# Performance work log

Hardware: AMD Instinct MI355X
Metric: run time of the kernel (lower is better)

The kernel has to match this reference:

```python
import jax, jax.numpy as jnp
import numpy as np

N_NODES = 100000

def gcn_conv(x, edge_index, W, b):
    # GCNConv with normalize=True and self-loops:
    # out = D^{-1/2} (A + I) D^{-1/2} (x W) + b
    h = x @ W                                   # [N, out]
    src, dst = edge_index[0], edge_index[1]
    deg = jax.ops.segment_sum(jnp.ones(src.shape[0], h.dtype), dst,
                              num_segments=N_NODES) + 1.0  # +1 for self loop
    dinv = jax.lax.rsqrt(deg)
    norm = dinv[src] * dinv[dst]                # [E]
    agg = jax.ops.segment_sum(h[src] * norm[:, None], dst,
                              num_segments=N_NODES)        # [N, out]
    agg = agg + h * (1.0 / deg)[:, None]        # self-loop term: norm_ii = 1/deg_i
    return agg + b


def setup_inputs() -> dict:
    key = jax.random.key(0)
    k0, k1, k2, k3 = jax.random.split(key, 4)
    N, E, F_IN, H, C = N_NODES, 1600000, 256, 128, 40
    x = jax.random.normal(k0, (N, F_IN), dtype=jnp.float32)
    edge_index = jax.random.randint(k1, (2, E), 0, N, dtype=jnp.int64)
    W1 = jax.random.normal(k2, (F_IN, H), dtype=jnp.float32) * (1.0 / np.sqrt(F_IN))
    b1 = jnp.zeros((H,), jnp.float32)
    W2 = jax.random.normal(k3, (H, C), dtype=jnp.float32) * (1.0 / np.sqrt(H))
    b2 = jnp.zeros((C,), jnp.float32)
    return {"x": x, "edge_index": edge_index, "W1": W1, "b1": b1, "W2": W2, "b2": b2}


def reference(x, edge_index, W1, b1, W2, b2):
    # layer 1 + ReLU (dropout = identity in eval mode)
    h = jax.nn.relu(gcn_conv(x, edge_index, W1, b1))
    # final layer (no activation)
    return gcn_conv(h, edge_index, W2, b2)
```

## Files before the change

kernel.cpp:

```cpp
#include <hip/hip_runtime.h>
#include <hip/hip_bf16.h>


#define FIN 256
#define HDIM 128
#define CDIM 40
#define CAP 8192
#define EC 8192

typedef __attribute__((ext_vector_type(8))) short bf16x8;
typedef __attribute__((ext_vector_type(4))) float f32x4;

__device__ inline short f2bf(float f) {
    unsigned u = __float_as_uint(f);
    unsigned r = (u + 0x7FFFu + ((u >> 16) & 1u)) >> 16;
    return (short)r;
}
__device__ inline float bflo(unsigned u) { return __uint_as_float(u << 16); }
__device__ inline float bfhi(unsigned u) { return __uint_as_float(u & 0xFFFF0000u); }

__global__ __launch_bounds__(1024) void p1_hist_k(const int* __restrict__ ei, int* __restrict__ mat,
                                                  int E, int NBUCK) {
    __shared__ int hist[512];
    for (int t = threadIdx.x; t < NBUCK; t += 1024) hist[t] = 0;
    __syncthreads();
    int e0 = blockIdx.x * EC;
#pragma unroll
    for (int k = 0; k < EC; k += 1024) {
        int e = e0 + k + threadIdx.x;
        if (e < E) atomicAdd(&hist[ei[E + e] >> 8], 1);
    }
    __syncthreads();
    for (int t = threadIdx.x; t < NBUCK; t += 1024) mat[blockIdx.x * NBUCK + t] = hist[t];
}

__global__ __launch_bounds__(64) void scan_cols_k(int* __restrict__ mat, int* __restrict__ bcnt,
                                                  int NB1, int NBUCK) {
    int b = blockIdx.x;
    int lane = threadIdx.x;
    int carry = b * CAP;
    for (int c0 = 0; c0 < NB1; c0 += 64) {
        int idx = c0 + lane;
        int v = (idx < NB1) ? mat[idx * NBUCK + b] : 0;
        int incl = v;
#pragma unroll
        for (int off = 1; off < 64; off <<= 1) {
            int t = __shfl_up(incl, off);
            if (lane >= off) incl += t;
        }
        if (idx < NB1) mat[idx * NBUCK + b] = carry + (incl - v);
        carry += __shfl(incl, 63);
    }
    if (lane == 0) bcnt[b] = carry - b * CAP;
}

__global__ __launch_bounds__(1024) void p1_scatter_k(const int* __restrict__ ei, const int* __restrict__ mat,
                                                     int* __restrict__ bmem, int E, int NBUCK) {
    __shared__ int base[512];
    for (int t = threadIdx.x; t < NBUCK; t += 1024) base[t] = mat[blockIdx.x * NBUCK + t];
    __syncthreads();
    int e0 = blockIdx.x * EC;
#pragma unroll
    for (int k = 0; k < EC; k += 1024) {
        int e = e0 + k + threadIdx.x;
        if (e < E) {
            int s = ei[e];
            int d = ei[E + e];
            int pos = atomicAdd(&base[d >> 8], 1);
            bmem[pos] = s | ((d & 255) << 20);
        }
    }
}

__global__ __launch_bounds__(256) void p2_build_k(const int* __restrict__ bmem, const int* __restrict__ bcnt,
                                                  int* __restrict__ csr, int2* __restrict__ nseg,
                                                  float* __restrict__ dinv, float* __restrict__ invd, int N) {
    __shared__ int hist[256], cur[256], sc[256];
    __shared__ int stage[CAP];
    const int b = blockIdx.x;
    const int tid = threadIdx.x;
    int cnt = bcnt[b];
    if (cnt > CAP) cnt = CAP;
    const int* src = bmem + b * CAP;
    hist[tid] = 0;
    __syncthreads();
    for (int j = tid; j < cnt; j += 256) atomicAdd(&hist[src[j] >> 20], 1);
    __syncthreads();
    int v = hist[tid];
    sc[tid] = v;
    __syncthreads();
    for (int off = 1; off < 256; off <<= 1) {
        int t = (tid >= off) ? sc[tid - off] : 0;
        __syncthreads();
        sc[tid] += t;
        __syncthreads();
    }
    int excl = sc[tid] - v;
    cur[tid] = excl;
    int i = b * 256 + tid;
    if (i < N) {
        nseg[i] = make_int2(b * CAP + excl, v);
        float dg = (float)(v + 1);
        dinv[i] = rsqrtf(dg);
        invd[i] = 1.0f / dg;
    }
    __syncthreads();
    for (int j = tid; j < cnt; j += 256) {
        int rec = src[j];
        int pos = atomicAdd(&cur[rec >> 20], 1);
        stage[pos] = rec & 0xFFFFF;
    }
    __syncthreads();
    int* dst = csr + b * CAP;
    for (int j = tid; j < cnt; j += 256) dst[j] = stage[j];
}

__global__ __launch_bounds__(256) void castW_k(const float* __restrict__ W1, const float* __restrict__ W2,
                                               short* __restrict__ W1T, short* __restrict__ W2T) {
    int idx = blockIdx.x * 256 + threadIdx.x;
    if (idx < FIN * HDIM) {
        int k = idx >> 7, n = idx & 127;
        W1T[n * FIN + k] = f2bf(W1[idx]);
    } else {
        int j = idx - FIN * HDIM;
        if (j < 48 * HDIM) {
            int c = j >> 7, k = j & 127;
            W2T[j] = (c < CDIM) ? f2bf(W2[k * CDIM + c]) : (short)0;
        }
    }
}

#define LDSTRIDE 40
__global__ __launch_bounds__(256) void gemm1_mfma_k(const float* __restrict__ X,
                                                    const short* __restrict__ W1T,
                                                    short* __restrict__ T1b, int N) {
    __shared__ short As[128 * LDSTRIDE];
    __shared__ short Bs[128 * LDSTRIDE];
    const int tid = threadIdx.x;
    const int lane = tid & 63;
    const int wid = tid >> 6;
    const int w0 = wid & 1, w1 = wid >> 1;
    const int quad = lane >> 4;
    const int l16 = lane & 15;
    const int rowbase = blockIdx.x * 128;
    const int sr = tid >> 1;
    const int sh = tid & 1;

    f32x4 acc[4][4];
#pragma unroll
    for (int a = 0; a < 4; a++)
#pragma unroll
        for (int b = 0; b < 4; b++) acc[a][b] = (f32x4){0.f, 0.f, 0.f, 0.f};

    const int arow = min(rowbase + sr, N - 1);
    const float* xsrc = X + (size_t)arow * FIN + sh * 16;
    const int4* bsrc = (const int4*)(W1T + (size_t)sr * FIN + sh * 16);

    for (int k0 = 0; k0 < FIN; k0 += 32) {
        float vals[16];
        *(float4*)&vals[0]  = *(const float4*)(xsrc + k0);
        *(float4*)&vals[4]  = *(const float4*)(xsrc + k0 + 4);
        *(float4*)&vals[8]  = *(const float4*)(xsrc + k0 + 8);
        *(float4*)&vals[12] = *(const float4*)(xsrc + k0 + 12);
        short tmp[16];
#pragma unroll
        for (int c = 0; c < 16; c++) tmp[c] = f2bf(vals[c]);
        ((int4*)&As[sr * LDSTRIDE + sh * 16])[0] = ((int4*)tmp)[0];
        ((int4*)&As[sr * LDSTRIDE + sh * 16])[1] = ((int4*)tmp)[1];
        int4 b0 = bsrc[k0 >> 3];
        int4 b1 = bsrc[(k0 >> 3) + 1];
        ((int4*)&Bs[sr * LDSTRIDE + sh * 16])[0] = b0;
        ((int4*)&Bs[sr * LDSTRIDE + sh * 16])[1] = b1;
        __syncthreads();

        bf16x8 afr[4], bfr[4];
#pragma unroll
        for (int mt = 0; mt < 4; mt++)
            afr[mt] = *(const bf16x8*)&As[(w1 * 64 + mt * 16 + l16) * LDSTRIDE + quad * 8];
#pragma unroll
        for (int nt = 0; nt < 4; nt++)
            bfr[nt] = *(const bf16x8*)&Bs[(w0 * 64 + nt * 16 + l16) * LDSTRIDE + quad * 8];
#pragma unroll
        for (int mt = 0; mt < 4; mt++)
#pragma unroll
            for (int nt = 0; nt < 4; nt++)
                acc[mt][nt] = __builtin_amdgcn_mfma_f32_16x16x32_bf16(afr[mt], bfr[nt], acc[mt][nt], 0, 0, 0);
        __syncthreads();
    }
#pragma unroll
    for (int mt = 0; mt < 4; mt++) {
#pragma unroll
        for (int r = 0; r < 4; r++) {
            int row = rowbase + w1 * 64 + mt * 16 + quad * 4 + r;
            if (row < N) {
#pragma unroll
                for (int nt = 0; nt < 4; nt++) {
                    int col = w0 * 64 + nt * 16 + l16;
                    T1b[(size_t)row * HDIM + col] = f2bf(acc[mt][nt][r]);
                }
            }
        }
    }
}

__global__ __launch_bounds__(256) void agg1_k(const short* __restrict__ T1b, const int2* __restrict__ nseg,
                                              const int* __restrict__ csr, const float* __restrict__ dinv,
                                              const float* __restrict__ invd, const float* __restrict__ b1,
                                              unsigned* __restrict__ Hb, int N) {
    const int lane = threadIdx.x & 63;
    const int quad = lane >> 4;
    const int ql = lane & 15;
    const int i = blockIdx.x * 4 + (threadIdx.x >> 6);
    if (i >= N) return;
    const int2 sg = nseg[i];
    const int e0 = sg.x, deg = sg.y;
    int sv = 0; float wv = 0.f;
    if (lane < deg) { sv = csr[e0 + lane]; wv = dinv[sv]; }

    const uint4* rowp = (const uint4*)T1b;
    float acc[8];
#pragma unroll
    for (int t = 0; t < 8; t++) acc[t] = 0.f;

    const int dmain = deg < 64 ? deg : 64;
    for (int j = 0; j < dmain; j += 16) {
        const int i0 = j + quad, i1 = j + 4 + quad, i2 = j + 8 + quad, i3 = j + 12 + quad;
        int s0 = __shfl(sv, i0); int s1 = __shfl(sv, i1);
        int s2 = __shfl(sv, i2); int s3 = __shfl(sv, i3);
        float w0 = __shfl(wv, i0); float w1 = __shfl(wv, i1);
        float w2 = __shfl(wv, i2); float w3 = __shfl(wv, i3);
        w0 = (i0 < dmain) ? w0 : 0.f;
        w1 = (i1 < dmain) ? w1 : 0.f;
        w2 = (i2 < dmain) ? w2 : 0.f;
        w3 = (i3 < dmain) ? w3 : 0.f;
        uint4 u0 = rowp[s0 * 16 + ql];
        uint4 u1 = rowp[s1 * 16 + ql];
        uint4 u2 = rowp[s2 * 16 + ql];
        uint4 u3 = rowp[s3 * 16 + ql];
        acc[0] += w0 * bflo(u0.x) + w1 * bflo(u1.x) + w2 * bflo(u2.x) + w3 * bflo(u3.x);
        acc[1] += w0 * bfhi(u0.x) + w1 * bfhi(u1.x) + w2 * bfhi(u2.x) + w3 * bfhi(u3.x);
        acc[2] += w0 * bflo(u0.y) + w1 * bflo(u1.y) + w2 * bflo(u2.y) + w3 * bflo(u3.y);
        acc[3] += w0 * bfhi(u0.y) + w1 * bfhi(u1.y) + w2 * bfhi(u2.y) + w3 * bfhi(u3.y);
        acc[4] += w0 * bflo(u0.z) + w1 * bflo(u1.z) + w2 * bflo(u2.z) + w3 * bflo(u3.z);
        acc[5] += w0 * bfhi(u0.z) + w1 * bfhi(u1.z) + w2 * bfhi(u2.z) + w3 * bfhi(u3.z);
        acc[6] += w0 * bflo(u0.w) + w1 * bflo(u1.w) + w2 * bflo(u2.w) + w3 * bflo(u3.w);
        acc[7] += w0 * bfhi(u0.w) + w1 * bfhi(u1.w) + w2 * bfhi(u2.w) + w3 * bfhi(u3.w);
    }
    const int eEnd = e0 + deg;
    for (int e = e0 + 64; e < eEnd; e += 4) {
        int idx = e + quad;
        int cl = idx < eEnd ? idx : eEnd - 1;
        int sj = csr[cl];
        float wj = (idx < eEnd) ? dinv[sj] : 0.f;
        uint4 u = rowp[sj * 16 + ql];
        acc[0] += wj * bflo(u.x); acc[1] += wj * bfhi(u.x);
        acc[2] += wj * bflo(u.y); acc[3] += wj * bfhi(u.y);
        acc[4] += wj * bflo(u.z); acc[5] += wj * bfhi(u.z);
        acc[6] += wj * bflo(u.w); acc[7] += wj * bfhi(u.w);
    }
#pragma unroll
    for (int t = 0; t < 8; t++) {
        acc[t] += __shfl_xor(acc[t], 16);
        acc[t] += __shfl_xor(acc[t], 32);
    }
    const float di = dinv[i], sf = invd[i];
    uint4 us = rowp[i * 16 + ql];
    float4 bA = *(const float4*)(b1 + ql * 8);
    float4 bB = *(const float4*)(b1 + ql * 8 + 4);
    float o0 = fmaxf(bA.x + sf * bflo(us.x) + di * acc[0], 0.f);
    float o1 = fmaxf(bA.y + sf * bfhi(us.x) + di * acc[1], 0.f);
    float o2 = fmaxf(bA.z + sf * bflo(us.y) + di * acc[2], 0.f);
    float o3 = fmaxf(bA.w + sf * bfhi(us.y) + di * acc[3], 0.f);
    float o4 = fmaxf(bB.x + sf * bflo(us.z) + di * acc[4], 0.f);
    float o5 = fmaxf(bB.y + sf * bfhi(us.z) + di * acc[5], 0.f);
    float o6 = fmaxf(bB.z + sf * bflo(us.w) + di * acc[6], 0.f);
    float o7 = fmaxf(bB.w + sf * bfhi(us.w) + di * acc[7], 0.f);
    uint4 pk;
    pk.x = ((unsigned)(unsigned short)f2bf(o0)) | (((unsigned)(unsigned short)f2bf(o1)) << 16);
    pk.y = ((unsigned)(unsigned short)f2bf(o2)) | (((unsigned)(unsigned short)f2bf(o3)) << 16);
    pk.z = ((unsigned)(unsigned short)f2bf(o4)) | (((unsigned)(unsigned short)f2bf(o5)) << 16);
    pk.w = ((unsigned)(unsigned short)f2bf(o6)) | (((unsigned)(unsigned short)f2bf(o7)) << 16);
    if (quad == 0) ((uint4*)(Hb + (size_t)i * 64))[ql] = pk;
}

__global__ __launch_bounds__(256) void gemm2_mfma_k(const short* __restrict__ Hb,
                                                    const short* __restrict__ W2T,
                                                    short* __restrict__ T2b, int N) {
    __shared__ short As[128 * LDSTRIDE];
    __shared__ short Bs[48 * LDSTRIDE];
    const int tid = threadIdx.x;
    const int lane = tid & 63;
    const int wid = tid >> 6;
    const int quad = lane >> 4;
    const int l16 = lane & 15;
    const int rowbase = blockIdx.x * 128;
    const int sr = tid >> 1;
    const int sh = tid & 1;

    f32x4 acc[2][3];
#pragma unroll
    for (int a = 0; a < 2; a++)
#pragma unroll
        for (int b = 0; b < 3; b++) acc[a][b] = (f32x4){0.f, 0.f, 0.f, 0.f};

    const int arow = min(rowbase + sr, N - 1);
    const int4* asrc = (const int4*)(Hb + (size_t)arow * HDIM + sh * 16);
    const int br = tid >> 1, bh = tid & 1;
    const int4* bsrc = (const int4*)(W2T + br * HDIM + bh * 16);

    for (int k0 = 0; k0 < HDIM; k0 += 32) {
        int4 a0 = asrc[k0 >> 3];
        int4 a1 = asrc[(k0 >> 3) + 1];
        ((int4*)&As[sr * LDSTRIDE + sh * 16])[0] = a0;
        ((int4*)&As[sr * LDSTRIDE + sh * 16])[1] = a1;
        if (tid < 96) {
            int4 b0 = bsrc[k0 >> 3];
            int4 b1 = bsrc[(k0 >> 3) + 1];
            ((int4*)&Bs[br * LDSTRIDE + bh * 16])[0] = b0;
            ((int4*)&Bs[br * LDSTRIDE + bh * 16])[1] = b1;
        }
        __syncthreads();
        bf16x8 afr[2], bfr[3];
#pragma unroll
        for (int mt = 0; mt < 2; mt++)
            afr[mt] = *(const bf16x8*)&As[(wid * 32 + mt * 16 + l16) * LDSTRIDE + quad * 8];
#pragma unroll
        for (int nt = 0; nt < 3; nt++)
            bfr[nt] = *(const bf16x8*)&Bs[(nt * 16 + l16) * LDSTRIDE + quad * 8];
#pragma unroll
        for (int mt = 0; mt < 2; mt++)
#pragma unroll
            for (int nt = 0; nt < 3; nt++)
                acc[mt][nt] = __builtin_amdgcn_mfma_f32_16x16x32_bf16(afr[mt], bfr[nt], acc[mt][nt], 0, 0, 0);
        __syncthreads();
    }
#pragma unroll
    for (int mt = 0; mt < 2; mt++) {
#pragma unroll
        for (int r = 0; r < 4; r++) {
            int row = rowbase + wid * 32 + mt * 16 + quad * 4 + r;
            if (row < N) {
#pragma unroll
                for (int nt = 0; nt < 3; nt++) {
                    int col = nt * 16 + l16;
                    T2b[(size_t)row * 48 + col] = f2bf(acc[mt][nt][r]);
                }
            }
        }
    }
}

__global__ __launch_bounds__(256) void agg2_k(const short* __restrict__ T2b, const int2* __restrict__ nseg,
                                              const int* __restrict__ csr, const float* __restrict__ dinv,
                                              const float* __restrict__ invd, const float* __restrict__ b2,
                                              float* __restrict__ OUT, int N) {
    const int lane = threadIdx.x & 63;
    const int oct = lane >> 3;
    const int olr = lane & 7;
    const int ol = olr < 6 ? olr : 5;
    const bool act = olr < 6;
    const int i = blockIdx.x * 4 + (threadIdx.x >> 6);
    if (i >= N) return;
    const int2 sg = nseg[i];
    const int e0 = sg.x, deg = sg.y;
    int sv = 0; float wv = 0.f;
    if (lane < deg) { sv = csr[e0 + lane]; wv = dinv[sv]; }

    const uint4* rowp = (const uint4*)T2b;
    float acc[8];
#pragma unroll
    for (int t = 0; t < 8; t++) acc[t] = 0.f;

    const int dmain = deg < 64 ? deg : 64;
    for (int j = 0; j < dmain; j += 16) {
        const int i0 = j + oct, i1 = j + 8 + oct;
        int s0 = __shfl(sv, i0); int s1 = __shfl(sv, i1);
        float w0 = __shfl(wv, i0); float w1 = __shfl(wv, i1);
        w0 = (i0 < dmain && act) ? w0 : 0.f;
        w1 = (i1 < dmain && act) ? w1 : 0.f;
        uint4 u0 = rowp[s0 * 6 + ol];
        uint4 u1 = rowp[s1 * 6 + ol];
        acc[0] += w0 * bflo(u0.x) + w1 * bflo(u1.x);
        acc[1] += w0 * bfhi(u0.x) + w1 * bfhi(u1.x);
        acc[2] += w0 * bflo(u0.y) + w1 * bflo(u1.y);
        acc[3] += w0 * bfhi(u0.y) + w1 * bfhi(u1.y);
        acc[4] += w0 * bflo(u0.z) + w1 * bflo(u1.z);
        acc[5] += w0 * bfhi(u0.z) + w1 * bfhi(u1.z);
        acc[6] += w0 * bflo(u0.w) + w1 * bflo(u1.w);
        acc[7] += w0 * bfhi(u0.w) + w1 * bfhi(u1.w);
    }
    const int eEnd = e0 + deg;
    for (int e = e0 + 64; e < eEnd; e += 8) {
        int idx = e + oct;
        int cl = idx < eEnd ? idx : eEnd - 1;
        int sj = csr[cl];
        float wj = (idx < eEnd && act) ? dinv[sj] : 0.f;
        uint4 u = rowp[sj * 6 + ol];
        acc[0] += wj * bflo(u.x); acc[1] += wj * bfhi(u.x);
        acc[2] += wj * bflo(u.y); acc[3] += wj * bfhi(u.y);
        acc[4] += wj * bflo(u.z); acc[5] += wj * bfhi(u.z);
        acc[6] += wj * bflo(u.w); acc[7] += wj * bfhi(u.w);
    }
#pragma unroll
    for (int t = 0; t < 8; t++) {
        acc[t] += __shfl_xor(acc[t], 8);
        acc[t] += __shfl_xor(acc[t], 16);
        acc[t] += __shfl_xor(acc[t], 32);
    }
    if (oct == 0 && olr < 5) {
        const float di = dinv[i], sf = invd[i];
        uint4 us = rowp[i * 6 + olr];
        float4 bA = *(const float4*)(b2 + olr * 8);
        float4 bB = *(const float4*)(b2 + olr * 8 + 4);
        float4 oA, oB;
        oA.x = bA.x + sf * bflo(us.x) + di * acc[0];
        oA.y = bA.y + sf * bfhi(us.x) + di * acc[1];
        oA.z = bA.z + sf * bflo(us.y) + di * acc[2];
        oA.w = bA.w + sf * bfhi(us.y) + di * acc[3];
        oB.x = bB.x + sf * bflo(us.z) + di * acc[4];
        oB.y = bB.y + sf * bfhi(us.z) + di * acc[5];
        oB.z = bB.z + sf * bflo(us.w) + di * acc[6];
        oB.w = bB.w + sf * bfhi(us.w) + di * acc[7];
        *(float4*)(OUT + (size_t)i * CDIM + olr * 8) = oA;
        *(float4*)(OUT + (size_t)i * CDIM + olr * 8 + 4) = oB;
    }
}

extern "C" void kernel_launch(void* const* d_in, const int* in_sizes, int n_in,
                              void* d_out, int out_size, void* d_ws, size_t ws_size,
                              hipStream_t stream) {
    const float* x   = (const float*)d_in[0];
    const int*   ei  = (const int*)d_in[1];
    const float* W1  = (const float*)d_in[2];
    const float* b1  = (const float*)d_in[3];
    const float* W2  = (const float*)d_in[4];
    const float* b2  = (const float*)d_in[5];
    float*       out = (float*)d_out;

    const int Hd  = in_sizes[3];
    const int Fin = in_sizes[2] / Hd;
    const int N   = in_sizes[0] / Fin;
    const int E   = in_sizes[1] / 2;

    const int NBUCK = (N + 255) / 256;
    const int NB1   = (E + EC - 1) / EC;

    char* base = (char*)d_ws;
    size_t off = 0;
    auto alloc = [&](size_t bytes) -> void* {
        void* p = base + off;
        off += (bytes + 255) & ~(size_t)255;
        return p;
    };
    size_t matB  = (size_t)NB1 * NBUCK * 4;
    size_t bmemB = (size_t)NBUCK * CAP * 4;
    size_t t1bB  = (size_t)N * HDIM * 2;
    size_t regA  = matB + 256 + bmemB;
    if (t1bB > regA) regA = t1bB;
    char* pA = (char*)alloc(regA);
    int*   mat  = (int*)pA;
    int*   bmem = (int*)(pA + ((matB + 255) & ~(size_t)255));
    short* t1b  = (short*)pA;

    int*      bcnt = (int*)alloc((size_t)NBUCK * 4);
    int*      csr  = (int*)alloc((size_t)NBUCK * CAP * 4);
    int2*     nseg = (int2*)alloc((size_t)N * 8);
    float*    dinv = (float*)alloc((size_t)N * 4);
    float*    invd = (float*)alloc((size_t)N * 4);
    short*    W1T  = (short*)alloc((size_t)HDIM * FIN * 2);
    short*    W2T  = (short*)alloc((size_t)48 * HDIM * 2);
    unsigned* hb   = (unsigned*)alloc((size_t)N * HDIM * 2);
    short*    t2b  = (short*)alloc((size_t)N * 48 * 2);

    p1_hist_k<<<NB1, 1024, 0, stream>>>(ei, mat, E, NBUCK);
    scan_cols_k<<<NBUCK, 64, 0, stream>>>(mat, bcnt, NB1, NBUCK);
    p1_scatter_k<<<NB1, 1024, 0, stream>>>(ei, mat, bmem, E, NBUCK);
    p2_build_k<<<NBUCK, 256, 0, stream>>>(bmem, bcnt, csr, nseg, dinv, invd, N);
    castW_k<<<(FIN * HDIM + 48 * HDIM + 255) / 256, 256, 0, stream>>>(W1, W2, W1T, W2T);

    gemm1_mfma_k<<<(N + 127) / 128, 256, 0, stream>>>(x, W1T, t1b, N);
    agg1_k<<<(N + 3) / 4, 256, 0, stream>>>(t1b, nseg, csr, dinv, invd, b1, hb, N);
    gemm2_mfma_k<<<(N + 127) / 128, 256, 0, stream>>>((const short*)hb, W2T, t2b, N);
    agg2_k<<<(N + 3) / 4, 256, 0, stream>>>(t2b, nseg, csr, dinv, invd, b2, out, N);
}
```

Before: 338.7 us.

## Fuse CSR build and weight cast into one cooperative kernel with grid syncs

Replaces five preprocessing launches (histogram, column scan, scatter, bucket build, weight cast) with one cooperative kernel that uses grid-wide syncs between phases. The edge chunking changes so that each of the NBUCK blocks handles E/NBUCK edges, 256 threads per block instead of 1024. This removes launch gaps and inter-kernel drains. In exchange it pays for grid.sync barriers, needs all 391 blocks with about 35KB of LDS each to be co-resident, and gives each block less parallelism for the histogram and scatter phases.

```diff
diff --git a/kernel.cpp b/kernel.cpp
--- a/kernel.cpp
+++ b/kernel.cpp
@@ -1,12 +1,14 @@
 #include <hip/hip_runtime.h>
 #include <hip/hip_bf16.h>
+#include <hip/hip_cooperative_groups.h>
+
+namespace cg = cooperative_groups;
 
 
 #define FIN 256
 #define HDIM 128
 #define CDIM 40
 #define CAP 8192
-#define EC 8192
 
 typedef __attribute__((ext_vector_type(8))) short bf16x8;
 typedef __attribute__((ext_vector_type(4))) float f32x4;
@@ -19,69 +21,75 @@
 __device__ inline float bflo(unsigned u) { return __uint_as_float(u << 16); }
 __device__ inline float bfhi(unsigned u) { return __uint_as_float(u & 0xFFFF0000u); }
 
-__global__ __launch_bounds__(1024) void p1_hist_k(const int* __restrict__ ei, int* __restrict__ mat,
-                                                  int E, int NBUCK) {
-    __shared__ int hist[512];
-    for (int t = threadIdx.x; t < NBUCK; t += 1024) hist[t] = 0;
-    __syncthreads();
-    int e0 = blockIdx.x * EC;
-#pragma unroll
-    for (int k = 0; k < EC; k += 1024) {
-        int e = e0 + k + threadIdx.x;
-        if (e < E) atomicAdd(&hist[ei[E + e] >> 8], 1);
-    }
-    __syncthreads();
-    for (int t = threadIdx.x; t < NBUCK; t += 1024) mat[blockIdx.x * NBUCK + t] = hist[t];
-}
-
-__global__ __launch_bounds__(64) void scan_cols_k(int* __restrict__ mat, int* __restrict__ bcnt,
-                                                  int NB1, int NBUCK) {
-    int b = blockIdx.x;
-    int lane = threadIdx.x;
-    int carry = b * CAP;
-    for (int c0 = 0; c0 < NB1; c0 += 64) {
-        int idx = c0 + lane;
-        int v = (idx < NB1) ? mat[idx * NBUCK + b] : 0;
-        int incl = v;
-#pragma unroll
-        for (int off = 1; off < 64; off <<= 1) {
-            int t = __shfl_up(incl, off);
-            if (lane >= off) incl += t;
+__global__ __launch_bounds__(256) void prep_k(const int* __restrict__ ei,
+                                              const float* __restrict__ W1, const float* __restrict__ W2,
+                                              int* __restrict__ mat, int* __restrict__ bmem,
+                                              int* __restrict__ bcnt, int* __restrict__ csr,
+                                              int2* __restrict__ nseg, float* __restrict__ dinv,
+                                              float* __restrict__ invd, short* __restrict__ W1T,
+                                              short* __restrict__ W2T, int E, int N, int NBUCK, int ec) {
+    cg::grid_group grid = cg::this_grid();
+    __shared__ int sm[768 + CAP];
+    const int tid = threadIdx.x;
+    const int b = blockIdx.x;
+    const int nb = gridDim.x;
+
+    for (int idx = b * 256 + tid; idx < FIN * HDIM + 48 * HDIM; idx += nb * 256) {
+        if (idx < FIN * HDIM) {
+            int k = idx >> 7, n = idx & 127;
+            W1T[n * FIN + k] = f2bf(W1[idx]);
+        } else {
+            int j = idx - FIN * HDIM;
+            int c = j >> 7, k = j & 127;
+            W2T[j] = (c < CDIM) ? f2bf(W2[k * CDIM + c]) : (short)0;
         }
-        if (idx < NB1) mat[idx * NBUCK + b] = carry + (incl - v);
-        carry += __shfl(incl, 63);
-    }
-    if (lane == 0) bcnt[b] = carry - b * CAP;
-}
-
-__global__ __launch_bounds__(1024) void p1_scatter_k(const int* __restrict__ ei, const int* __restrict__ mat,
-                                                     int* __restrict__ bmem, int E, int NBUCK) {
-    __shared__ int base[512];
-    for (int t = threadIdx.x; t < NBUCK; t += 1024) base[t] = mat[blockIdx.x * NBUCK + t];
-    __syncthreads();
-    int e0 = blockIdx.x * EC;
-#pragma unroll
-    for (int k = 0; k < EC; k += 1024) {
-        int e = e0 + k + threadIdx.x;
-        if (e < E) {
-            int s = ei[e];
-            int d = ei[E + e];
-            int pos = atomicAdd(&base[d >> 8], 1);
-            bmem[pos] = s | ((d & 255) << 20);
+    }
+
+    for (int t = tid; t < NBUCK; t += 256) sm[t] = 0;
+    __syncthreads();
+    const int e0 = b * ec;
+    const int e1 = min(E, e0 + ec);
+    for (int e = e0 + tid; e < e1; e += 256) atomicAdd(&sm[ei[E + e] >> 8], 1);
+    __syncthreads();
+    for (int t = tid; t < NBUCK; t += 256) mat[b * NBUCK + t] = sm[t];
+    grid.sync();
+
+    if (tid < 64) {
+        int carry = b * CAP;
+        for (int c0 = 0; c0 < nb; c0 += 64) {
+            int idx = c0 + tid;
+            int v = (idx < nb) ? mat[idx * NBUCK + b] : 0;
+            int incl = v;
+#pragma unroll
+            for (int off = 1; off < 64; off <<= 1) {
+                int t = __shfl_up(incl, off);
+                if (tid >= off) incl += t;
+            }
+            if (idx < nb) mat[idx * NBUCK + b] = carry + (incl - v);
+            carry += __shfl(incl, 63);
         }
-    }
-}
-
-__global__ __launch_bounds__(256) void p2_build_k(const int* __restrict__ bmem, const int* __restrict__ bcnt,
-                                                  int* __restrict__ csr, int2* __restrict__ nseg,
-                                                  float* __restrict__ dinv, float* __restrict__ invd, int N) {
-    __shared__ int hist[256], cur[256], sc[256];
-    __shared__ int stage[CAP];
-    const int b = blockIdx.x;
-    const int tid = threadIdx.x;
+        if (tid == 0) bcnt[b] = carry - b * CAP;
+    }
+    grid.sync();
+
+    for (int t = tid; t < NBUCK; t += 256) sm[t] = mat[b * NBUCK + t];
+    __syncthreads();
+    for (int e = e0 + tid; e < e1; e += 256) {
+        int s = ei[e];
+        int d = ei[E + e];
+        int pos = atomicAdd(&sm[d >> 8], 1);
+        bmem[pos] = s | ((d & 255) << 20);
+    }
+    grid.sync();
+
+    int* hist  = sm;
+    int* cur   = sm + 256;
+    int* sc    = sm + 512;
+    int* stage = sm + 768;
     int cnt = bcnt[b];
     if (cnt > CAP) cnt = CAP;
     const int* src = bmem + b * CAP;
+    __syncthreads();
     hist[tid] = 0;
     __syncthreads();
     for (int j = tid; j < cnt; j += 256) atomicAdd(&hist[src[j] >> 20], 1);
@@ -113,21 +121,6 @@
     __syncthreads();
     int* dst = csr + b * CAP;
     for (int j = tid; j < cnt; j += 256) dst[j] = stage[j];
-}
-
-__global__ __launch_bounds__(256) void castW_k(const float* __restrict__ W1, const float* __restrict__ W2,
-                                               short* __restrict__ W1T, short* __restrict__ W2T) {
-    int idx = blockIdx.x * 256 + threadIdx.x;
-    if (idx < FIN * HDIM) {
-        int k = idx >> 7, n = idx & 127;
-        W1T[n * FIN + k] = f2bf(W1[idx]);
-    } else {
-        int j = idx - FIN * HDIM;
-        if (j < 48 * HDIM) {
-            int c = j >> 7, k = j & 127;
-            W2T[j] = (c < CDIM) ? f2bf(W2[k * CDIM + c]) : (short)0;
-        }
-    }
 }
 
 #define LDSTRIDE 40
@@ -439,11 +432,11 @@
 
     const int Hd  = in_sizes[3];
     const int Fin = in_sizes[2] / Hd;
-    const int N   = in_sizes[0] / Fin;
-    const int E   = in_sizes[1] / 2;
-
-    const int NBUCK = (N + 255) / 256;
-    const int NB1   = (E + EC - 1) / EC;
+    int N   = in_sizes[0] / Fin;
+    int E   = in_sizes[1] / 2;
+
+    int NBUCK = (N + 255) / 256;
+    int ec    = (E + NBUCK - 1) / NBUCK;
 
     char* base = (char*)d_ws;
     size_t off = 0;
@@ -452,10 +445,10 @@
         off += (bytes + 255) & ~(size_t)255;
         return p;
     };
-    size_t matB  = (size_t)NB1 * NBUCK * 4;
+    size_t matB  = (size_t)NBUCK * NBUCK * 4;
     size_t bmemB = (size_t)NBUCK * CAP * 4;
     size_t t1bB  = (size_t)N * HDIM * 2;
-    size_t regA  = matB + 256 + bmemB;
+    size_t regA  = ((matB + 255) & ~(size_t)255) + bmemB;
     if (t1bB > regA) regA = t1bB;
     char* pA = (char*)alloc(regA);
     int*   mat  = (int*)pA;
@@ -472,11 +465,10 @@
     unsigned* hb   = (unsigned*)alloc((size_t)N * HDIM * 2);
     short*    t2b  = (short*)alloc((size_t)N * 48 * 2);
 
-    p1_hist_k<<<NB1, 1024, 0, stream>>>(ei, mat, E, NBUCK);
-    scan_cols_k<<<NBUCK, 64, 0, stream>>>(mat, bcnt, NB1, NBUCK);
-    p1_scatter_k<<<NB1, 1024, 0, stream>>>(ei, mat, bmem, E, NBUCK);
-    p2_build_k<<<NBUCK, 256, 0, stream>>>(bmem, bcnt, csr, nseg, dinv, invd, N);
-    castW_k<<<(FIN * HDIM + 48 * HDIM + 255) / 256, 256, 0, stream>>>(W1, W2, W1T, W2T);
+    void* args[] = {(void*)&ei, (void*)&W1, (void*)&W2, (void*)&mat, (void*)&bmem,
+                    (void*)&bcnt, (void*)&csr, (void*)&nseg, (void*)&dinv, (void*)&invd,
+                    (void*)&W1T, (void*)&W2T, (void*)&E, (void*)&N, (void*)&NBUCK, (void*)&ec};
+    hipLaunchCooperativeKernel((void*)prep_k, dim3(NBUCK), dim3(256), args, 0, stream);
 
     gemm1_mfma_k<<<(N + 127) / 128, 256, 0, stream>>>(x, W1T, t1b, N);
     agg1_k<<<(N + 3) / 4, 256, 0, stream>>>(t1b, nseg, csr, dinv, invd, b1, hb, N);
```

Measured after the change: 505.8 us. 1.49x slower.

## Merge CSR histogram, scan and scatter into one atomic-reserve kernel; fold weight cast

Applied to the files above, without the earlier changes.

Replaces the three-kernel bucket sort (per-block histogram, column scan, scatter) with one kernel that builds a local histogram and reserves slots in each bucket through global atomics on a zeroed counter array. The weight cast/transpose moves into the p2_build kernel as a grid-stride loop. Together these cut launches and drop the histogram matrix traffic. The aggregation kernels also switch to packed float2 accumulators, which may let the compiler emit packed FMA. Within-bucket edge order becomes nondeterministic, so float summation order can vary between runs.

```diff
diff --git a/kernel.cpp b/kernel.cpp
--- a/kernel.cpp
+++ b/kernel.cpp
@@ -10,6 +10,7 @@
 
 typedef __attribute__((ext_vector_type(8))) short bf16x8;
 typedef __attribute__((ext_vector_type(4))) float f32x4;
+typedef __attribute__((ext_vector_type(2))) float f32x2;
 
 __device__ inline short f2bf(float f) {
     unsigned u = __float_as_uint(f);
@@ -18,67 +19,51 @@
 }
 __device__ inline float bflo(unsigned u) { return __uint_as_float(u << 16); }
 __device__ inline float bfhi(unsigned u) { return __uint_as_float(u & 0xFFFF0000u); }
-
-__global__ __launch_bounds__(1024) void p1_hist_k(const int* __restrict__ ei, int* __restrict__ mat,
-                                                  int E, int NBUCK) {
+__device__ inline f32x2 unpk(unsigned u) { return (f32x2){bflo(u), bfhi(u)}; }
+
+__global__ __launch_bounds__(1024) void scatter_k(const int* __restrict__ ei, int* __restrict__ gcnt,
+                                                  int* __restrict__ bmem, int E, int NBUCK) {
     __shared__ int hist[512];
-    for (int t = threadIdx.x; t < NBUCK; t += 1024) hist[t] = 0;
-    __syncthreads();
-    int e0 = blockIdx.x * EC;
-#pragma unroll
-    for (int k = 0; k < EC; k += 1024) {
-        int e = e0 + k + threadIdx.x;
-        if (e < E) atomicAdd(&hist[ei[E + e] >> 8], 1);
-    }
-    __syncthreads();
-    for (int t = threadIdx.x; t < NBUCK; t += 1024) mat[blockIdx.x * NBUCK + t] = hist[t];
-}
-
-__global__ __launch_bounds__(64) void scan_cols_k(int* __restrict__ mat, int* __restrict__ bcnt,
-                                                  int NB1, int NBUCK) {
-    int b = blockIdx.x;
-    int lane = threadIdx.x;
-    int carry = b * CAP;
-    for (int c0 = 0; c0 < NB1; c0 += 64) {
-        int idx = c0 + lane;
-        int v = (idx < NB1) ? mat[idx * NBUCK + b] : 0;
-        int incl = v;
-#pragma unroll
-        for (int off = 1; off < 64; off <<= 1) {
-            int t = __shfl_up(incl, off);
-            if (lane >= off) incl += t;
-        }
-        if (idx < NB1) mat[idx * NBUCK + b] = carry + (incl - v);
-        carry += __shfl(incl, 63);
-    }
-    if (lane == 0) bcnt[b] = carry - b * CAP;
-}
-
-__global__ __launch_bounds__(1024) void p1_scatter_k(const int* __restrict__ ei, const int* __restrict__ mat,
-                                                     int* __restrict__ bmem, int E, int NBUCK) {
     __shared__ int base[512];
-    for (int t = threadIdx.x; t < NBUCK; t += 1024) base[t] = mat[blockIdx.x * NBUCK + t];
-    __syncthreads();
-    int e0 = blockIdx.x * EC;
-#pragma unroll
-    for (int k = 0; k < EC; k += 1024) {
-        int e = e0 + k + threadIdx.x;
-        if (e < E) {
-            int s = ei[e];
-            int d = ei[E + e];
-            int pos = atomicAdd(&base[d >> 8], 1);
-            bmem[pos] = s | ((d & 255) << 20);
-        }
+    const int tid = threadIdx.x;
+    for (int t = tid; t < NBUCK; t += 1024) hist[t] = 0;
+    __syncthreads();
+    const int e0 = blockIdx.x * EC;
+    const int e1 = min(E, e0 + EC);
+    for (int e = e0 + tid; e < e1; e += 1024) atomicAdd(&hist[ei[E + e] >> 8], 1);
+    __syncthreads();
+    for (int t = tid; t < NBUCK; t += 1024) base[t] = atomicAdd(&gcnt[t], hist[t]);
+    __syncthreads();
+    for (int e = e0 + tid; e < e1; e += 1024) {
+        int s = ei[e];
+        int d = ei[E + e];
+        int b = d >> 8;
+        int pos = atomicAdd(&base[b], 1);
+        bmem[b * CAP + pos] = s | ((d & 255) << 20);
     }
 }
 
 __global__ __launch_bounds__(256) void p2_build_k(const int* __restrict__ bmem, const int* __restrict__ bcnt,
                                                   int* __restrict__ csr, int2* __restrict__ nseg,
-                                                  float* __restrict__ dinv, float* __restrict__ invd, int N) {
+                                                  float* __restrict__ dinv, float* __restrict__ invd,
+                                                  const float* __restrict__ W1, const float* __restrict__ W2,
+                                                  short* __restrict__ W1T, short* __restrict__ W2T, int N) {
     __shared__ int hist[256], cur[256], sc[256];
     __shared__ int stage[CAP];
     const int b = blockIdx.x;
     const int tid = threadIdx.x;
+
+    for (int idx = b * 256 + tid; idx < FIN * HDIM + 48 * HDIM; idx += gridDim.x * 256) {
+        if (idx < FIN * HDIM) {
+            int k = idx >> 7, n = idx & 127;
+            W1T[n * FIN + k] = f2bf(W1[idx]);
+        } else {
+            int j = idx - FIN * HDIM;
+            int c = j >> 7, k = j & 127;
+            W2T[j] = (c < CDIM) ? f2bf(W2[k * CDIM + c]) : (short)0;
+        }
+    }
+
     int cnt = bcnt[b];
     if (cnt > CAP) cnt = CAP;
     const int* src = bmem + b * CAP;
@@ -113,21 +98,6 @@
     __syncthreads();
     int* dst = csr + b * CAP;
     for (int j = tid; j < cnt; j += 256) dst[j] = stage[j];
-}
-
-__global__ __launch_bounds__(256) void castW_k(const float* __restrict__ W1, const float* __restrict__ W2,
-                                               short* __restrict__ W1T, short* __restrict__ W2T) {
-    int idx = blockIdx.x * 256 + threadIdx.x;
-    if (idx < FIN * HDIM) {
-        int k = idx >> 7, n = idx & 127;
-        W1T[n * FIN + k] = f2bf(W1[idx]);
-    } else {
-        int j = idx - FIN * HDIM;
-        if (j < 48 * HDIM) {
-            int c = j >> 7, k = j & 127;
-            W2T[j] = (c < CDIM) ? f2bf(W2[k * CDIM + c]) : (short)0;
-        }
-    }
 }
 
 #define LDSTRIDE 40
@@ -218,9 +188,9 @@
     if (lane < deg) { sv = csr[e0 + lane]; wv = dinv[sv]; }
 
     const uint4* rowp = (const uint4*)T1b;
-    float acc[8];
-#pragma unroll
-    for (int t = 0; t < 8; t++) acc[t] = 0.f;
+    f32x2 acc[4];
+#pragma unroll
+    for (int t = 0; t < 4; t++) acc[t] = (f32x2){0.f, 0.f};
 
     const int dmain = deg < 64 ? deg : 64;
     for (int j = 0; j < dmain; j += 16) {
@@ -237,14 +207,11 @@
         uint4 u1 = rowp[s1 * 16 + ql];
         uint4 u2 = rowp[s2 * 16 + ql];
         uint4 u3 = rowp[s3 * 16 + ql];
-        acc[0] += w0 * bflo(u0.x) + w1 * bflo(u1.x) + w2 * bflo(u2.x) + w3 * bflo(u3.x);
-        acc[1] += w0 * bfhi(u0.x) + w1 * bfhi(u1.x) + w2 * bfhi(u2.x) + w3 * bfhi(u3.x);
-        acc[2] += w0 * bflo(u0.y) + w1 * bflo(u1.y) + w2 * bflo(u2.y) + w3 * bflo(u3.y);
-        acc[3] += w0 * bfhi(u0.y) + w1 * bfhi(u1.y) + w2 * bfhi(u2.y) + w3 * bfhi(u3.y);
-        acc[4] += w0 * bflo(u0.z) + w1 * bflo(u1.z) + w2 * bflo(u2.z) + w3 * bflo(u3.z);
-        acc[5] += w0 * bfhi(u0.z) + w1 * bfhi(u1.z) + w2 * bfhi(u2.z) + w3 * bfhi(u3.z);
-        acc[6] += w0 * bflo(u0.w) + w1 * bflo(u1.w) + w2 * bflo(u2.w) + w3 * bflo(u3.w);
-        acc[7] += w0 * bfhi(u0.w) + w1 * bfhi(u1.w) + w2 * bfhi(u2.w) + w3 * bfhi(u3.w);
+        f32x2 W0 = (f32x2){w0, w0}, W1v = (f32x2){w1, w1}, W2v = (f32x2){w2, w2}, W3v = (f32x2){w3, w3};
+        acc[0] += W0 * unpk(u0.x) + W1v * unpk(u1.x) + W2v * unpk(u2.x) + W3v * unpk(u3.x);
+        acc[1] += W0 * unpk(u0.y) + W1v * unpk(u1.y) + W2v * unpk(u2.y) + W3v * unpk(u3.y);
+        acc[2] += W0 * unpk(u0.z) + W1v * unpk(u1.z) + W2v * unpk(u2.z) + W3v * unpk(u3.z);
+        acc[3] += W0 * unpk(u0.w) + W1v * unpk(u1.w) + W2v * unpk(u2.w) + W3v * unpk(u3.w);
     }
     const int eEnd = e0 + deg;
     for (int e = e0 + 64; e < eEnd; e += 4) {
@@ -253,28 +220,29 @@
         int sj = csr[cl];
         float wj = (idx < eEnd) ? dinv[sj] : 0.f;
         uint4 u = rowp[sj * 16 + ql];
-        acc[0] += wj * bflo(u.x); acc[1] += wj * bfhi(u.x);
-        acc[2] += wj * bflo(u.y); acc[3] += wj * bfhi(u.y);
-        acc[4] += wj * bflo(u.z); acc[5] += wj * bfhi(u.z);
-        acc[6] += wj * bflo(u.w); acc[7] += wj * bfhi(u.w);
-    }
-#pragma unroll
-    for (int t = 0; t < 8; t++) {
-        acc[t] += __shfl_xor(acc[t], 16);
-        acc[t] += __shfl_xor(acc[t], 32);
+        f32x2 Wj = (f32x2){wj, wj};
+        acc[0] += Wj * unpk(u.x);
+        acc[1] += Wj * unpk(u.y);
+        acc[2] += Wj * unpk(u.z);
+        acc[3] += Wj * unpk(u.w);
+    }
+#pragma unroll
+    for (int t = 0; t < 4; t++) {
+        acc[t].x += __shfl_xor(acc[t].x, 16); acc[t].y += __shfl_xor(acc[t].y, 16);
+        acc[t].x += __shfl_xor(acc[t].x, 32); acc[t].y += __shfl_xor(acc[t].y, 32);
     }
     const float di = dinv[i], sf = invd[i];
     uint4 us = rowp[i * 16 + ql];
     float4 bA = *(const float4*)(b1 + ql * 8);
     float4 bB = *(const float4*)(b1 + ql * 8 + 4);
-    float o0 = fmaxf(bA.x + sf * bflo(us.x) + di * acc[0], 0.f);
-    float o1 = fmaxf(bA.y + sf * bfhi(us.x) + di * acc[1], 0.f);
-    float o2 = fmaxf(bA.z + sf * bflo(us.y) + di * acc[2], 0.f);
-    float o3 = fmaxf(bA.w + sf * bfhi(us.y) + di * acc[3], 0.f);
-    float o4 = fmaxf(bB.x + sf * bflo(us.z) + di * acc[4], 0.f);
-    float o5 = fmaxf(bB.y + sf * bfhi(us.z) + di * acc[5], 0.f);
-    float o6 = fmaxf(bB.z + sf * bflo(us.w) + di * acc[6], 0.f);
-    float o7 = fmaxf(bB.w + sf * bfhi(us.w) + di * acc[7], 0.f);
+    float o0 = fmaxf(bA.x + sf * bflo(us.x) + di * acc[0].x, 0.f);
+    float o1 = fmaxf(bA.y + sf * bfhi(us.x) + di * acc[0].y, 0.f);
+    float o2 = fmaxf(bA.z + sf * bflo(us.y) + di * acc[1].x, 0.f);
+    float o3 = fmaxf(bA.w + sf * bfhi(us.y) + di * acc[1].y, 0.f);
+    float o4 = fmaxf(bB.x + sf * bflo(us.z) + di * acc[2].x, 0.f);
+    float o5 = fmaxf(bB.y + sf * bfhi(us.z) + di * acc[2].y, 0.f);
+    float o6 = fmaxf(bB.z + sf * bflo(us.w) + di * acc[3].x, 0.f);
+    float o7 = fmaxf(bB.w + sf * bfhi(us.w) + di * acc[3].y, 0.f);
     uint4 pk;
     pk.x = ((unsigned)(unsigned short)f2bf(o0)) | (((unsigned)(unsigned short)f2bf(o1)) << 16);
     pk.y = ((unsigned)(unsigned short)f2bf(o2)) | (((unsigned)(unsigned short)f2bf(o3)) << 16);
@@ -367,9 +335,9 @@
     if (lane < deg) { sv = csr[e0 + lane]; wv = dinv[sv]; }
 
     const uint4* rowp = (const uint4*)T2b;
-    float acc[8];
-#pragma unroll
-    for (int t = 0; t < 8; t++) acc[t] = 0.f;
+    f32x2 acc[4];
+#pragma unroll
+    for (int t = 0; t < 4; t++) acc[t] = (f32x2){0.f, 0.f};
 
     const int dmain = deg < 64 ? deg : 64;
     for (int j = 0; j < dmain; j += 16) {
@@ -380,14 +348,11 @@
         w1 = (i1 < dmain && act) ? w1 : 0.f;
         uint4 u0 = rowp[s0 * 6 + ol];
         uint4 u1 = rowp[s1 * 6 + ol];
-        acc[0] += w0 * bflo(u0.x) + w1 * bflo(u1.x);
-        acc[1] += w0 * bfhi(u0.x) + w1 * bfhi(u1.x);
-        acc[2] += w0 * bflo(u0.y) + w1 * bflo(u1.y);
-        acc[3] += w0 * bfhi(u0.y) + w1 * bfhi(u1.y);
-        acc[4] += w0 * bflo(u0.z) + w1 * bflo(u1.z);
-        acc[5] += w0 * bfhi(u0.z) + w1 * bfhi(u1.z);
-        acc[6] += w0 * bflo(u0.w) + w1 * bflo(u1.w);
-        acc[7] += w0 * bfhi(u0.w) + w1 * bfhi(u1.w);
+        f32x2 W0 = (f32x2){w0, w0}, W1v = (f32x2){w1, w1};
+        acc[0] += W0 * unpk(u0.x) + W1v * unpk(u1.x);
+        acc[1] += W0 * unpk(u0.y) + W1v * unpk(u1.y);
+        acc[2] += W0 * unpk(u0.z) + W1v * unpk(u1.z);
+        acc[3] += W0 * unpk(u0.w) + W1v * unpk(u1.w);
     }
     const int eEnd = e0 + deg;
     for (int e = e0 + 64; e < eEnd; e += 8) {
@@ -396,16 +361,17 @@
         int sj = csr[cl];
         float wj = (idx < eEnd && act) ? dinv[sj] : 0.f;
         uint4 u = rowp[sj * 6 + ol];
-        acc[0] += wj * bflo(u.x); acc[1] += wj * bfhi(u.x);
-        acc[2] += wj * bflo(u.y); acc[3] += wj * bfhi(u.y);
-        acc[4] += wj * bflo(u.z); acc[5] += wj * bfhi(u.z);
-        acc[6] += wj * bflo(u.w); acc[7] += wj * bfhi(u.w);
-    }
-#pragma unroll
-    for (int t = 0; t < 8; t++) {
-        acc[t] += __shfl_xor(acc[t], 8);
-        acc[t] += __shfl_xor(acc[t], 16);
-        acc[t] += __shfl_xor(acc[t], 32);
+        f32x2 Wj = (f32x2){wj, wj};
+        acc[0] += Wj * unpk(u.x);
+        acc[1] += Wj * unpk(u.y);
+        acc[2] += Wj * unpk(u.z);
+        acc[3] += Wj * unpk(u.w);
+    }
+#pragma unroll
+    for (int t = 0; t < 4; t++) {
+        acc[t].x += __shfl_xor(acc[t].x, 8);  acc[t].y += __shfl_xor(acc[t].y, 8);
+        acc[t].x += __shfl_xor(acc[t].x, 16); acc[t].y += __shfl_xor(acc[t].y, 16);
+        acc[t].x += __shfl_xor(acc[t].x, 32); acc[t].y += __shfl_xor(acc[t].y, 32);
     }
     if (oct == 0 && olr < 5) {
         const float di = dinv[i], sf = invd[i];
@@ -413,14 +379,14 @@
         float4 bA = *(const float4*)(b2 + olr * 8);
         float4 bB = *(const float4*)(b2 + olr * 8 + 4);
         float4 oA, oB;
-        oA.x = bA.x + sf * bflo(us.x) + di * acc[0];
-        oA.y = bA.y + sf * bfhi(us.x) + di * acc[1];
-        oA.z = bA.z + sf * bflo(us.y) + di * acc[2];
-        oA.w = bA.w + sf * bfhi(us.y) + di * acc[3];
-        oB.x = bB.x + sf * bflo(us.z) + di * acc[4];
-        oB.y = bB.y + sf * bfhi(us.z) + di * acc[5];
-        oB.z = bB.z + sf * bflo(us.w) + di * acc[6];
-        oB.w = bB.w + sf * bfhi(us.w) + di * acc[7];
+        oA.x = bA.x + sf * bflo(us.x) + di * acc[0].x;
+        oA.y = bA.y + sf * bfhi(us.x) + di * acc[0].y;
+        oA.z = bA.z + sf * bflo(us.y) + di * acc[1].x;
+        oA.w = bA.w + sf * bfhi(us.y) + di * acc[1].y;
+        oB.x = bB.x + sf * bflo(us.z) + di * acc[2].x;
+        oB.y = bB.y + sf * bfhi(us.z) + di * acc[2].y;
+        oB.z = bB.z + sf * bflo(us.w) + di * acc[3].x;
+        oB.w = bB.w + sf * bfhi(us.w) + di * acc[3].y;
         *(float4*)(OUT + (size_t)i * CDIM + olr * 8) = oA;
         *(float4*)(OUT + (size_t)i * CDIM + olr * 8 + 4) = oB;
     }
@@ -452,17 +418,14 @@
         off += (bytes + 255) & ~(size_t)255;
         return p;
     };
-    size_t matB  = (size_t)NB1 * NBUCK * 4;
     size_t bmemB = (size_t)NBUCK * CAP * 4;
     size_t t1bB  = (size_t)N * HDIM * 2;
-    size_t regA  = matB + 256 + bmemB;
-    if (t1bB > regA) regA = t1bB;
+    size_t regA  = bmemB > t1bB ? bmemB : t1bB;
     char* pA = (char*)alloc(regA);
-    int*   mat  = (int*)pA;
-    int*   bmem = (int*)(pA + ((matB + 255) & ~(size_t)255));
+    int*   bmem = (int*)pA;
     short* t1b  = (short*)pA;
 
-    int*      bcnt = (int*)alloc((size_t)NBUCK * 4);
+    int*      gcnt = (int*)alloc((size_t)NBUCK * 4);
     int*      csr  = (int*)alloc((size_t)NBUCK * CAP * 4);
     int2*     nseg = (int2*)alloc((size_t)N * 8);
     float*    dinv = (float*)alloc((size_t)N * 4);
@@ -472,11 +435,9 @@
     unsigned* hb   = (unsigned*)alloc((size_t)N * HDIM * 2);
     short*    t2b  = (short*)alloc((size_t)N * 48 * 2);
 
-    p1_hist_k<<<NB1, 1024, 0, stream>>>(ei, mat, E, NBUCK);
-    scan_cols_k<<<NBUCK, 64, 0, stream>>>(mat, bcnt, NB1, NBUCK);
-    p1_scatter_k<<<NB1, 1024, 0, stream>>>(ei, mat, bmem, E, NBUCK);
-    p2_build_k<<<NBUCK, 256, 0, stream>>>(bmem, bcnt, csr, nseg, dinv, invd, N);
-    castW_k<<<(FIN * HDIM + 48 * HDIM + 255) / 256, 256, 0, stream>>>(W1, W2, W1T, W2T);
+    hipMemsetAsync(gcnt, 0, (size_t)NBUCK * 4, stream);
+    scatter_k<<<NB1, 1024, 0, stream>>>(ei, gcnt, bmem, E, NBUCK);
+    p2_build_k<<<NBUCK, 256, 0, stream>>>(bmem, gcnt, csr, nseg, dinv, invd, W1, W2, W1T, W2T, N);
 
     gemm1_mfma_k<<<(N + 127) / 128, 256, 0, stream>>>(x, W1T, t1b, N);
     agg1_k<<<(N + 3) / 4, 256, 0, stream>>>(t1b, nseg, csr, dinv, invd, b1, hb, N);
```

After: 332.6 us. About the same (-1.8%).
